# Kernel tuning notes

Measured on AMD Instinct MI355X. Metric: run time of the kernel, lower is better.

Reference implementation:

```python
import jax, jax.numpy as jnp
import numpy as np

B, S, D = 2, 2048, 1024   # batch, seq, token_dim
H, E = 16, 64             # heads, embedding_size per head


def setup_inputs() -> dict:
    key = jax.random.key(0)
    ks = jax.random.split(key, 5)
    x = jax.random.normal(ks[0], (B, S, D), dtype=jnp.float32)
    attention_mask = jnp.ones((B, S), dtype=jnp.int32)  # accepted but unused, as in source
    # torch.rand -> uniform [0,1)
    w_queries = jax.random.uniform(ks[1], (H, D, E), dtype=jnp.float32)
    w_keys = jax.random.uniform(ks[2], (H, D, E), dtype=jnp.float32)
    w_values = jax.random.uniform(ks[3], (H, D, E), dtype=jnp.float32)
    w_agg = jax.random.uniform(ks[4], (H * E, D), dtype=jnp.float32)
    return {"x": x, "attention_mask": attention_mask, "w_queries": w_queries,
            "w_keys": w_keys, "w_values": w_values, "w_agg": w_agg}


def reference(x, attention_mask, w_queries, w_keys, w_values, w_agg):
    # Batched over all heads at once (original loops in Python per head).
    q = jnp.einsum('bsd,hde->bhse', x, w_queries)  # [B,H,S,E]
    k = jnp.einsum('bsd,hde->bhse', x, w_keys)
    v = jnp.einsum('bsd,hde->bhse', x, w_values)
    scores = jnp.einsum('bhse,bhte->bhst', q, k) / jnp.sqrt(jnp.float32(E))  # [B,H,S,S]
    # NOTE: source applies softmax over dim=1 of the per-head [B,S,S] scores,
    # i.e. over the QUERY axis (axis=2 here), not the usual key axis.
    attn = jax.nn.softmax(scores, axis=2)
    heads = jnp.einsum('bhst,bhte->bhse', attn, v)  # [B,H,S,E]
    # concat along last dim in head order -> [B,S,H*E]
    multi = jnp.transpose(heads, (0, 2, 1, 3)).reshape(B, S, H * E)
    return multi @ w_agg  # [B,S,D]
```

## Files before the change

kernel.cpp:

```cpp
#include <hip/hip_runtime.h>
#include <hip/hip_bf16.h>


typedef __attribute__((ext_vector_type(8))) short bf16x8;
typedef __attribute__((ext_vector_type(4))) float f32x4;

#define C1 0.18033688011112042f

__device__ __forceinline__ unsigned short f2bf(float f){
  union { __hip_bfloat16 h; unsigned short u; } cv;
  cv.h = __float2bfloat16(f);
  return cv.u;
}
__device__ __forceinline__ unsigned int pk2(float a, float b){
  union { __hip_bfloat162 h; unsigned int u; } cv;
  cv.h = __float22bfloat162_rn(make_float2(a, b));
  return cv.u;
}
__device__ __forceinline__ unsigned long long pack4(float a, float b, float c, float d){
  return (unsigned long long)pk2(a, b) | ((unsigned long long)pk2(c, d) << 32);
}
__device__ __forceinline__ float bf2f(unsigned short u){
  unsigned int x = ((unsigned int)u) << 16;
  return __builtin_bit_cast(float, x);
}

__device__ __forceinline__ void swap32(unsigned a, unsigned b, unsigned &x, unsigned &y){
#if __has_builtin(__builtin_amdgcn_permlane32_swap)
  auto r = __builtin_amdgcn_permlane32_swap(a, b, false, false);
  x = r[0]; y = r[1];
#else
  int lane = threadIdx.x & 63;
  unsigned as = __shfl_xor((int)a, 32), bs = __shfl_xor((int)b, 32);
  x = (lane & 32) ? bs : a;
  y = (lane & 32) ? b : as;
#endif
}
__device__ __forceinline__ void swap16(unsigned a, unsigned b, unsigned &x, unsigned &y){
#if __has_builtin(__builtin_amdgcn_permlane16_swap)
  auto r = __builtin_amdgcn_permlane16_swap(a, b, false, false);
  x = r[0]; y = r[1];
#else
  int lane = threadIdx.x & 63;
  unsigned as = __shfl_xor((int)a, 16), bs = __shfl_xor((int)b, 16);
  x = (lane & 16) ? bs : a;
  y = (lane & 16) ? b : as;
#endif
}

#define GLOAD16(SRC, DST)                                                        \
  __builtin_amdgcn_global_load_lds(                                              \
      (const __attribute__((address_space(1))) void*)(SRC),                      \
      (__attribute__((address_space(3))) void*)(DST), 16, 0, 0)

__global__ void k_cvt_x(const float* __restrict__ in, unsigned short* __restrict__ out){
  int i = (blockIdx.x * 256 + threadIdx.x) * 4;
  float4 v = *reinterpret_cast<const float4*>(in + i);
  *reinterpret_cast<unsigned long long*>(out + i) = pack4(v.x, v.y, v.z, v.w);
}

__global__ __launch_bounds__(256) void k_cvt_w3t(const float* __restrict__ wq,
                                                 const float* __restrict__ wk,
                                                 const float* __restrict__ wv,
                                                 unsigned short* __restrict__ out){
  __shared__ unsigned short T[64][72];
  const int z = blockIdx.z;
  const float* w = ((z == 0) ? wq : ((z == 1) ? wk : wv)) + ((size_t)blockIdx.y << 16);
  const int d0 = blockIdx.x * 64;
  const int r = threadIdx.x >> 2, c0 = (threadIdx.x & 3) << 4;
  const float* src = w + ((size_t)(d0 + r) << 6) + c0;
#pragma unroll
  for (int i = 0; i < 4; ++i){
    float4 v = *(const float4*)(src + 4 * i);
    T[r][c0 + 4 * i + 0] = f2bf(v.x);
    T[r][c0 + 4 * i + 1] = f2bf(v.y);
    T[r][c0 + 4 * i + 2] = f2bf(v.z);
    T[r][c0 + 4 * i + 3] = f2bf(v.w);
  }
  __syncthreads();
  const int e = threadIdx.x >> 2, k0 = (threadIdx.x & 3) << 4;
  union { unsigned short s[8]; bf16x8 v; } u0, u1;
#pragma unroll
  for (int k = 0; k < 8; ++k){ u0.s[k] = T[k0 + k][e]; u1.s[k] = T[k0 + 8 + k][e]; }
  unsigned short* dst = out + ((size_t)z << 20) + (((size_t)blockIdx.y * 64 + e) << 10) + d0 + k0;
  *(bf16x8*)dst = u0.v;
  *(bf16x8*)(dst + 8) = u1.v;
}

__global__ __launch_bounds__(256) void k_cvt_waggt(const float* __restrict__ w,
                                                   unsigned short* __restrict__ out){
  __shared__ unsigned short T[64][72];
  const int d0 = blockIdx.x * 64, he0 = blockIdx.y * 64;
  const int r = threadIdx.x >> 2, c0 = (threadIdx.x & 3) << 4;
  const float* src = w + ((size_t)(he0 + r) << 10) + d0 + c0;
#pragma unroll
  for (int i = 0; i < 4; ++i){
    float4 v = *(const float4*)(src + 4 * i);
    T[r][c0 + 4 * i + 0] = f2bf(v.x);
    T[r][c0 + 4 * i + 1] = f2bf(v.y);
    T[r][c0 + 4 * i + 2] = f2bf(v.z);
    T[r][c0 + 4 * i + 3] = f2bf(v.w);
  }
  __syncthreads();
  const int d = threadIdx.x >> 2, k0 = (threadIdx.x & 3) << 4;
  union { unsigned short s[8]; bf16x8 v; } u0, u1;
#pragma unroll
  for (int k = 0; k < 8; ++k){ u0.s[k] = T[k0 + k][d]; u1.s[k] = T[k0 + 8 + k][d]; }
  unsigned short* dst = out + ((size_t)(d0 + d) << 11) + he0 + k0;
  *(bf16x8*)dst = u0.v;
  *(bf16x8*)(dst + 8) = u1.v;
  *(bf16x8*)(dst + 1024) = u0.v;
  *(bf16x8*)(dst + 1032) = u1.v;
}

__global__ __launch_bounds__(256) void k_proj(const unsigned short* __restrict__ Wall,
                                              const unsigned short* __restrict__ Xb,
                                              unsigned short* __restrict__ Qb,
                                              unsigned short* __restrict__ Kb,
                                              unsigned short* __restrict__ Vt){
  __shared__ __align__(16) unsigned short lds[2][2][4096];
  const int z = blockIdx.z;
  const unsigned short* Wt = Wall + ((size_t)z << 20);
  const int t = threadIdx.x;
  const int w = t >> 6, lane = t & 63, g = lane >> 4, cl = lane & 15;
  const int wn = w >> 1, wm = w & 1;
  const int n0 = blockIdx.x * 128, m0 = blockIdx.y * 128;

  const int rowS = t & 127;
  const unsigned short* sA = Wt + (size_t)(n0 + rowS) * 1024 + (t >> 7) * 8;
  const unsigned short* sB = Xb + (size_t)(m0 + rowS) * 1024 + (t >> 7) * 8;

  f32x4 acc[4][4];
#pragma unroll
  for (int i = 0; i < 4; ++i)
#pragma unroll
    for (int j = 0; j < 4; ++j) acc[i][j] = f32x4{0.f, 0.f, 0.f, 0.f};

  GLOAD16(sA,      &lds[0][0][t * 8]);
  GLOAD16(sA + 16, &lds[0][0][t * 8 + 2048]);
  GLOAD16(sB,      &lds[0][1][t * 8]);
  GLOAD16(sB + 16, &lds[0][1][t * 8 + 2048]);
  __syncthreads();

#pragma unroll 2
  for (int kt = 0; kt < 32; ++kt){
    const int cur = kt & 1;
    if (kt < 31){
      const unsigned short* nA = sA + (kt + 1) * 32;
      const unsigned short* nB = sB + (kt + 1) * 32;
      GLOAD16(nA,      &lds[cur ^ 1][0][t * 8]);
      GLOAD16(nA + 16, &lds[cur ^ 1][0][t * 8 + 2048]);
      GLOAD16(nB,      &lds[cur ^ 1][1][t * 8]);
      GLOAD16(nB + 16, &lds[cur ^ 1][1][t * 8 + 2048]);
    }
    const unsigned short* la = &lds[cur][0][g * 1024];
    const unsigned short* lb = &lds[cur][1][g * 1024];
    bf16x8 af[4], bq[4];
#pragma unroll
    for (int i = 0; i < 4; ++i) af[i] = *(const bf16x8*)(la + (wn * 64 + i * 16 + cl) * 8);
#pragma unroll
    for (int j = 0; j < 4; ++j) bq[j] = *(const bf16x8*)(lb + (wm * 64 + j * 16 + cl) * 8);
#pragma unroll
    for (int i = 0; i < 4; ++i)
#pragma unroll
      for (int j = 0; j < 4; ++j)
        acc[i][j] = __builtin_amdgcn_mfma_f32_16x16x32_bf16(af[i], bq[j], acc[i][j], 0, 0, 0);
    __syncthreads();
  }

  const float scale = (z == 0) ? C1 : 1.f;
#pragma unroll
  for (int i = 0; i < 4; ++i)
#pragma unroll
    for (int j = 0; j < 4; ++j)
#pragma unroll
      for (int jj = 0; jj < 4; ++jj) acc[i][j][jj] *= scale;

  if (z < 2){
    unsigned short* outp = (z == 0) ? Qb : Kb;
#pragma unroll
    for (int i = 0; i < 4; ++i)
#pragma unroll
      for (int j = 0; j < 4; ++j){
        int m = m0 + wm * 64 + 16 * j + cl;
        int n = n0 + wn * 64 + 16 * i + 4 * g;
        *reinterpret_cast<unsigned long long*>(outp + (size_t)m * 1024 + n) =
            pack4(acc[i][j][0], acc[i][j][1], acc[i][j][2], acc[i][j][3]);
      }
  } else {
    int b = m0 >> 11;
#pragma unroll
    for (int i = 0; i < 4; ++i)
#pragma unroll
      for (int j = 0; j < 4; ++j){
        int c2 = (m0 & 2047) + wm * 64 + 16 * j + cl;
        int nb = b * 1024 + n0 + wn * 64 + 16 * i + 4 * g;
#pragma unroll
        for (int jj = 0; jj < 4; ++jj)
          Vt[(size_t)(nb + jj) * 2048 + c2] = f2bf(acc[i][j][jj]);
      }
  }
}

__global__ __launch_bounds__(256) void k_agg(const unsigned short* __restrict__ Wa,
                                             const unsigned short* __restrict__ Hd,
                                             float* __restrict__ outp){
  __shared__ __align__(16) unsigned short lds[2][6144];
  const int t = threadIdx.x;
  const int w = t >> 6, lane = t & 63, g = lane >> 4, cl = lane & 15;
  const int wn = w >> 1, wm = w & 1;
  const int n0 = blockIdx.x * 64, m0 = blockIdx.y * 128;

  const unsigned short* sA  = Wa + (size_t)(n0 + (t & 63)) * 2048 + (t >> 6) * 8;
  const unsigned short* sB1 = Hd + (size_t)(m0 + (t & 127)) * 2048 + (t >> 7) * 8;
  unsigned short* dA0  = &lds[0][0]    + t * 8;
  unsigned short* dB10 = &lds[0][2048] + t * 8;

  f32x4 acc[2][4];
#pragma unroll
  for (int j = 0; j < 2; ++j)
#pragma unroll
    for (int i = 0; i < 4; ++i) acc[j][i] = f32x4{0.f, 0.f, 0.f, 0.f};

  GLOAD16(sA,       dA0);
  GLOAD16(sB1,      dB10);
  GLOAD16(sB1 + 16, dB10 + 2048);
  __syncthreads();

#pragma unroll 2
  for (int kt = 0; kt < 64; ++kt){
    const int cur = kt & 1;
    if (kt < 63){
      const unsigned short* nA = sA  + (kt + 1) * 32;
      const unsigned short* nB = sB1 + (kt + 1) * 32;
      GLOAD16(nA,      dA0  + (cur ^ 1) * 6144);
      GLOAD16(nB,      dB10 + (cur ^ 1) * 6144);
      GLOAD16(nB + 16, dB10 + (cur ^ 1) * 6144 + 2048);
    }
    const unsigned short* la = &lds[cur][0];
    const unsigned short* lb = &lds[cur][2048];
    bf16x8 af[2], bq[4];
#pragma unroll
    for (int j = 0; j < 2; ++j) af[j] = *(const bf16x8*)(la + g * 512 + (wn * 32 + j * 16 + cl) * 8);
#pragma unroll
    for (int i = 0; i < 4; ++i) bq[i] = *(const bf16x8*)(lb + g * 1024 + (wm * 64 + i * 16 + cl) * 8);
#pragma unroll
    for (int j = 0; j < 2; ++j)
#pragma unroll
      for (int i = 0; i < 4; ++i)
        acc[j][i] = __builtin_amdgcn_mfma_f32_16x16x32_bf16(af[j], bq[i], acc[j][i], 0, 0, 0);
    __syncthreads();
  }
#pragma unroll
  for (int j = 0; j < 2; ++j)
#pragma unroll
    for (int i = 0; i < 4; ++i){
      int m = m0 + wm * 64 + 16 * i + cl;
      int n = n0 + wn * 32 + 16 * j + 4 * g;
      *reinterpret_cast<f32x4*>(outp + (size_t)m * 1024 + n) = acc[j][i];
    }
}

__global__ __launch_bounds__(256, 4) void k_stats(const unsigned short* __restrict__ Qb,
                                                  const unsigned short* __restrict__ Kb,
                                                  float* __restrict__ mp,
                                                  float* __restrict__ lp){
  __shared__ __align__(16) unsigned short Qs[2][64][64];
  const int B = blockIdx.x;
  const int xcd = B & 7, rest = B >> 3;
  const int tx = rest & 7, gi = rest >> 3;
  const int grp = xcd + 8 * gi;
  const int bh = grp & 31, z = grp >> 5;
  const int b = bh >> 4, h = bh & 15;
  const int w = threadIdx.x >> 6, lane = threadIdx.x & 63;
  const int g = lane >> 4, cl = lane & 15;
  const int t0 = tx * 256 + w * 64;

  const unsigned short* kp = Kb + (size_t)(b * 2048 + t0 + cl) * 1024 + h * 64 + g * 8;
  bf16x8 a[4][2];
#pragma unroll
  for (int ti = 0; ti < 4; ++ti){
    a[ti][0] = *(const bf16x8*)(kp + (size_t)ti * 16 * 1024);
    a[ti][1] = *(const bf16x8*)(kp + (size_t)ti * 16 * 1024 + 32);
  }

  const int r0 = threadIdx.x >> 3, sl = threadIdx.x & 7;
  const unsigned short* qsrc = Qb + (size_t)(b * 2048 + z * 512 + r0) * 1024 + h * 64
                               + ((sl ^ (r0 & 7)) * 8);
  unsigned short* qdst0 = &Qs[0][0][0] + threadIdx.x * 8;

  const int e0 = (g ^ (cl & 7)) * 8;
  const int e1 = ((g + 4) ^ (cl & 7)) * 8;

  float m[16], l[16];
#pragma unroll
  for (int i = 0; i < 16; ++i){ m[i] = -3.0e38f; l[i] = 0.f; }

  GLOAD16(qsrc,             qdst0);
  GLOAD16(qsrc + 32 * 1024, qdst0 + 2048);
  __syncthreads();
  for (int c = 0; c < 8; ++c){
    const int buf = c & 1;
    if (c < 7){
      const unsigned short* s2 = qsrc + (size_t)(c + 1) * 64 * 1024;
      unsigned short* d2 = qdst0 + (buf ^ 1) * 4096;
      GLOAD16(s2,             d2);
      GLOAD16(s2 + 32 * 1024, d2 + 2048);
    }
#pragma unroll
    for (int st = 0; st < 4; ++st){
      const unsigned short* qrow = &Qs[buf][st * 16 + cl][0];
      bf16x8 b0 = *(const bf16x8*)(qrow + e0);
      bf16x8 b1 = *(const bf16x8*)(qrow + e1);
#pragma unroll
      for (int ti = 0; ti < 4; ++ti){
        f32x4 zz = {0.f, 0.f, 0.f, 0.f};
        f32x4 d = __builtin_amdgcn_mfma_f32_16x16x32_bf16(a[ti][0], b0, zz, 0, 0, 0);
        d = __builtin_amdgcn_mfma_f32_16x16x32_bf16(a[ti][1], b1, d, 0, 0, 0);
#pragma unroll
        for (int j = 0; j < 4; ++j) m[ti * 4 + j] = fmaxf(m[ti * 4 + j], d[j]);
      }
    }
    __syncthreads();
  }
#pragma unroll
  for (int off = 1; off < 16; off <<= 1)
#pragma unroll
    for (int i = 0; i < 16; ++i) m[i] = fmaxf(m[i], __shfl_xor(m[i], off));

  GLOAD16(qsrc,             qdst0);
  GLOAD16(qsrc + 32 * 1024, qdst0 + 2048);
  __syncthreads();
  for (int c = 0; c < 8; ++c){
    const int buf = c & 1;
    if (c < 7){
      const unsigned short* s2 = qsrc + (size_t)(c + 1) * 64 * 1024;
      unsigned short* d2 = qdst0 + (buf ^ 1) * 4096;
      GLOAD16(s2,             d2);
      GLOAD16(s2 + 32 * 1024, d2 + 2048);
    }
#pragma unroll
    for (int st = 0; st < 4; ++st){
      const unsigned short* qrow = &Qs[buf][st * 16 + cl][0];
      bf16x8 b0 = *(const bf16x8*)(qrow + e0);
      bf16x8 b1 = *(const bf16x8*)(qrow + e1);
#pragma unroll
      for (int ti = 0; ti < 4; ++ti){
        f32x4 zz = {0.f, 0.f, 0.f, 0.f};
        f32x4 d = __builtin_amdgcn_mfma_f32_16x16x32_bf16(a[ti][0], b0, zz, 0, 0, 0);
        d = __builtin_amdgcn_mfma_f32_16x16x32_bf16(a[ti][1], b1, d, 0, 0, 0);
#pragma unroll
        for (int j = 0; j < 4; ++j) l[ti * 4 + j] += exp2f(d[j] - m[ti * 4 + j]);
      }
    }
    __syncthreads();
  }
#pragma unroll
  for (int off = 1; off < 16; off <<= 1)
#pragma unroll
    for (int i = 0; i < 16; ++i) l[i] += __shfl_xor(l[i], off);

  if (cl == 0){
    size_t base = ((size_t)z * 32 + bh) * 2048 + t0;
#pragma unroll
    for (int ti = 0; ti < 4; ++ti){
      f32x4 mv = {m[ti * 4 + 0], m[ti * 4 + 1], m[ti * 4 + 2], m[ti * 4 + 3]};
      f32x4 lv = {l[ti * 4 + 0], l[ti * 4 + 1], l[ti * 4 + 2], l[ti * 4 + 3]};
      *(f32x4*)(mp + base + ti * 16 + 4 * g) = mv;
      *(f32x4*)(lp + base + ti * 16 + 4 * g) = lv;
    }
  }
}

__global__ void k_mcomb(const float* __restrict__ mp, const float* __restrict__ lp,
                        float* __restrict__ m2, float* __restrict__ rl){
  int i = blockIdx.x * 256 + threadIdx.x;
  float m0 = mp[i], m1 = mp[65536 + i], m2v = mp[131072 + i], m3 = mp[196608 + i];
  float l0 = lp[i], l1 = lp[65536 + i], l2 = lp[131072 + i], l3 = lp[196608 + i];
  float m = fmaxf(fmaxf(m0, m1), fmaxf(m2v, m3));
  float l = l0 * exp2f(m0 - m) + l1 * exp2f(m1 - m)
          + l2 * exp2f(m2v - m) + l3 * exp2f(m3 - m);
  m2[i] = m;
  rl[i] = 1.f / l;
}

__global__ void k_scale_v(unsigned short* __restrict__ Vt, const float* __restrict__ rl){
  int row = blockIdx.x;
  int b = row >> 10, h = (row >> 6) & 15;
  int t = threadIdx.x * 8;
  const float* r = rl + (size_t)(b * 16 + h) * 2048 + t;
  unsigned short* p = Vt + (size_t)row * 2048 + t;
  bf16x8 v = *(const bf16x8*)p;
  f32x4 r0 = *(const f32x4*)r;
  f32x4 r1 = *(const f32x4*)(r + 4);
  float f[8];
#pragma unroll
  for (int j = 0; j < 8; ++j) f[j] = bf2f((unsigned short)v[j]);
#pragma unroll
  for (int j = 0; j < 4; ++j){ f[j] *= r0[j]; f[4 + j] *= r1[j]; }
  unsigned long long* q = (unsigned long long*)p;
  q[0] = pack4(f[0], f[1], f[2], f[3]);
  q[1] = pack4(f[4], f[5], f[6], f[7]);
}

__global__ __launch_bounds__(256, 4) void k_attn(const unsigned short* __restrict__ Qb,
                                                 const unsigned short* __restrict__ Kb,
                                                 const unsigned short* __restrict__ Vt,
                                                 const float* __restrict__ m2,
                                                 unsigned short* __restrict__ Hd){
  __shared__ __align__(16) unsigned short KsL[2 * 64 * 64];
  __shared__ __align__(16) unsigned short VsL[2 * 64 * 64];
  __shared__ __align__(16) float Ms[1024];
  const int B = blockIdx.x;
  const int xcd = B & 7, rest = B >> 3;
  const int sx = rest & 15, gi = rest >> 4;
  const int grp = xcd + 8 * gi;
  const int bh = grp & 31, z = grp >> 5;
  const int b = bh >> 4, h = bh & 15;
  const int lane = threadIdx.x & 63;
  const int g = lane >> 4, cl = lane & 15;
  const int s0w = sx * 128 + (threadIdx.x >> 6) * 32;
  const int tbase = z * 1024;

  {
    int i = threadIdx.x * 4;
    *(f32x4*)&Ms[i] = *(const f32x4*)(m2 + (size_t)bh * 2048 + tbase + i);
  }

  bf16x8 q[2][2];
#pragma unroll
  for (int ss = 0; ss < 2; ++ss){
    const unsigned short* qp = Qb + (size_t)(b * 2048 + s0w + ss * 16 + cl) * 1024 + h * 64 + g * 8;
    q[ss][0] = *(const bf16x8*)(qp);
    q[ss][1] = *(const bf16x8*)(qp + 32);
  }
  f32x4 acc[4][2];
#pragma unroll
  for (int i = 0; i < 4; ++i)
#pragma unroll
    for (int ss = 0; ss < 2; ++ss) acc[i][ss] = f32x4{0.f, 0.f, 0.f, 0.f};

  const int srow = threadIdx.x >> 3;
  const int sseg = ((threadIdx.x & 7) ^ (srow & 7)) * 8;
  const unsigned short* kStage = Kb + (size_t)(b * 2048 + tbase + srow) * 1024 + h * 64 + sseg;
  const unsigned short* vStage = Vt + (size_t)(b * 1024 + h * 64 + srow) * 2048 + tbase + sseg;
  unsigned short* kDst = &KsL[0] + threadIdx.x * 8;
  unsigned short* vDst = &VsL[0] + threadIdx.x * 8;

  const int eK = (g ^ (cl & 7)) * 8;
  const int eK2 = ((g + 4) ^ (cl & 7)) * 8;

#define ASTAGE(c, buf) {                                                          \
    const unsigned short* ks_ = kStage + (size_t)(c) * 64 * 1024;                 \
    const unsigned short* vs_ = vStage + (c) * 64;                                \
    unsigned short* kd_ = kDst + (buf) * 4096;                                    \
    unsigned short* vd_ = vDst + (buf) * 4096;                                    \
    GLOAD16(ks_,             kd_);                                                \
    GLOAD16(ks_ + 32 * 1024, kd_ + 2048);                                         \
    GLOAD16(vs_,             vd_);                                                \
    GLOAD16(vs_ + (size_t)32 * 2048, vd_ + 2048); }

  ASTAGE(0, 0);
  __syncthreads();

  for (int c = 0; c < 16; ++c){
    const int buf = c & 1;
    if (c < 15) ASTAGE(c + 1, buf ^ 1);
    const unsigned short* Kbuf = &KsL[0] + buf * 4096;
    const unsigned short* Vbuf = &VsL[0] + buf * 4096;
#pragma unroll
    for (int sc = 0; sc < 2; ++sc){
      const unsigned short* kr0 = Kbuf + (sc * 32 + cl) * 64;
      const unsigned short* kr1 = Kbuf + (sc * 32 + 16 + cl) * 64;
      bf16x8 a00 = *(const bf16x8*)(kr0 + eK);
      bf16x8 a01 = *(const bf16x8*)(kr0 + eK2);
      bf16x8 a10 = *(const bf16x8*)(kr1 + eK);
      bf16x8 a11 = *(const bf16x8*)(kr1 + eK2);
      f32x4 mv0 = *(const f32x4*)&Ms[c * 64 + sc * 32 + 4 * g];
      f32x4 mv1 = *(const f32x4*)&Ms[c * 64 + sc * 32 + 16 + 4 * g];

      bf16x8 pb[2];
#pragma unroll
      for (int ss = 0; ss < 2; ++ss){
        f32x4 zz = {0.f, 0.f, 0.f, 0.f};
        __builtin_amdgcn_s_setprio(1);
        f32x4 d0 = __builtin_amdgcn_mfma_f32_16x16x32_bf16(a00, q[ss][0], zz, 0, 0, 0);
        d0 = __builtin_amdgcn_mfma_f32_16x16x32_bf16(a01, q[ss][1], d0, 0, 0, 0);
        f32x4 d1 = __builtin_amdgcn_mfma_f32_16x16x32_bf16(a10, q[ss][0], zz, 0, 0, 0);
        d1 = __builtin_amdgcn_mfma_f32_16x16x32_bf16(a11, q[ss][1], d1, 0, 0, 0);
        __builtin_amdgcn_s_setprio(0);
        unsigned w00 = pk2(exp2f(d0[0] - mv0[0]), exp2f(d0[1] - mv0[1]));
        unsigned w01 = pk2(exp2f(d0[2] - mv0[2]), exp2f(d0[3] - mv0[3]));
        unsigned w10 = pk2(exp2f(d1[0] - mv1[0]), exp2f(d1[1] - mv1[1]));
        unsigned w11 = pk2(exp2f(d1[2] - mv1[2]), exp2f(d1[3] - mv1[3]));
        unsigned sa0, sb0, sa1, sb1, W0, W1, W2, W3;
        swap32(w00, w10, sa0, sb0);
        swap32(w01, w11, sa1, sb1);
        swap16(sa0, sb0, W0, W2);
        swap16(sa1, sb1, W1, W3);
        union { unsigned u[4]; bf16x8 v; } fr;
        fr.u[0] = W0; fr.u[1] = W1; fr.u[2] = W2; fr.u[3] = W3;
        pb[ss] = fr.v;
      }
      __builtin_amdgcn_s_setprio(1);
#pragma unroll
      for (int i = 0; i < 4; ++i){
        bf16x8 av = *(const bf16x8*)(Vbuf + (16 * i + cl) * 64 + ((sc * 4 + g) ^ (cl & 7)) * 8);
        acc[i][0] = __builtin_amdgcn_mfma_f32_16x16x32_bf16(av, pb[0], acc[i][0], 0, 0, 0);
        acc[i][1] = __builtin_amdgcn_mfma_f32_16x16x32_bf16(av, pb[1], acc[i][1], 0, 0, 0);
      }
      __builtin_amdgcn_s_setprio(0);
    }
    __syncthreads();
  }
#undef ASTAGE
#pragma unroll
  for (int i = 0; i < 4; ++i)
#pragma unroll
    for (int ss = 0; ss < 2; ++ss){
      *reinterpret_cast<unsigned long long*>(
          Hd + (size_t)(b * 2048 + s0w + ss * 16 + cl) * 2048 + z * 1024 + h * 64 + 16 * i + 4 * g) =
          pack4(acc[i][ss][0], acc[i][ss][1], acc[i][ss][2], acc[i][ss][3]);
    }
}

extern "C" void kernel_launch(void* const* d_in, const int* in_sizes, int n_in,
                              void* d_out, int out_size, void* d_ws, size_t ws_size,
                              hipStream_t stream) {
  const float* x    = (const float*)d_in[0];
  const float* wq   = (const float*)d_in[2];
  const float* wk   = (const float*)d_in[3];
  const float* wv   = (const float*)d_in[4];
  const float* wagg = (const float*)d_in[5];
  float* outp = (float*)d_out;

  char* ws = (char*)d_ws;
  unsigned short* Xb  = (unsigned short*)(ws);
  unsigned short* Hd  = (unsigned short*)(ws);
  unsigned short* Wall= (unsigned short*)(ws + 16777216);
  float* mp = (float*)(ws + 16777216);
  float* lp = (float*)(ws + 17825792);
  float* m2 = (float*)(ws + 18874368);
  float* rl = (float*)(ws + 19136512);
  unsigned short* Wat = (unsigned short*)(ws + 23068672);
  unsigned short* Qb  = (unsigned short*)(ws + 27262976);
  unsigned short* Kb  = (unsigned short*)(ws + 35651584);
  unsigned short* Vt  = (unsigned short*)(ws + 44040192);

  k_cvt_x    <<<dim3(4096),       dim3(256), 0, stream>>>(x, Xb);
  k_cvt_w3t  <<<dim3(16, 16, 3),  dim3(256), 0, stream>>>(wq, wk, wv, Wall);
  k_cvt_waggt<<<dim3(16, 16),     dim3(256), 0, stream>>>(wagg, Wat);

  k_proj<<<dim3(8, 32, 3), dim3(256), 0, stream>>>(Wall, Xb, Qb, Kb, Vt);

  k_stats  <<<dim3(1024), dim3(256), 0, stream>>>(Qb, Kb, mp, lp);
  k_mcomb  <<<dim3(256),  dim3(256), 0, stream>>>(mp, lp, m2, rl);
  k_scale_v<<<dim3(2048), dim3(256), 0, stream>>>(Vt, rl);

  k_attn<<<dim3(1024), dim3(256), 0, stream>>>(Qb, Kb, Vt, m2, Hd);
  k_agg <<<dim3(16, 32), dim3(256), 0, stream>>>(Wat, Hd, outp);
}
```

Measured before the change: 245.4 us.

## Merge conversion kernels into one launch and fold max subtraction into MFMA accumulator

Combines the three fp32-to-bf16 conversion and transpose kernels into a single k_prep launch dispatched by block index, saving two kernel launches and the gaps between them. In the attention kernel, the softmax max is negated when loaded into shared memory and passed as the initial MFMA accumulator, so the subtraction happens inside the matrix op and is no longer a separate per-element subtract before exp2. The added branching in the merged prep kernel is small, but mixing block types in one grid may slightly change how work spreads across compute units.

```diff
diff --git a/kernel.cpp b/kernel.cpp
--- a/kernel.cpp
+++ b/kernel.cpp
@@ -53,64 +53,71 @@
       (const __attribute__((address_space(1))) void*)(SRC),                      \
       (__attribute__((address_space(3))) void*)(DST), 16, 0, 0)
 
-__global__ void k_cvt_x(const float* __restrict__ in, unsigned short* __restrict__ out){
-  int i = (blockIdx.x * 256 + threadIdx.x) * 4;
-  float4 v = *reinterpret_cast<const float4*>(in + i);
-  *reinterpret_cast<unsigned long long*>(out + i) = pack4(v.x, v.y, v.z, v.w);
-}
-
-__global__ __launch_bounds__(256) void k_cvt_w3t(const float* __restrict__ wq,
-                                                 const float* __restrict__ wk,
-                                                 const float* __restrict__ wv,
-                                                 unsigned short* __restrict__ out){
+__global__ __launch_bounds__(256) void k_prep(const float* __restrict__ x,
+                                              const float* __restrict__ wq,
+                                              const float* __restrict__ wk,
+                                              const float* __restrict__ wv,
+                                              const float* __restrict__ wagg,
+                                              unsigned short* __restrict__ Xb,
+                                              unsigned short* __restrict__ Wall,
+                                              unsigned short* __restrict__ Wat){
   __shared__ unsigned short T[64][72];
-  const int z = blockIdx.z;
-  const float* w = ((z == 0) ? wq : ((z == 1) ? wk : wv)) + ((size_t)blockIdx.y << 16);
-  const int d0 = blockIdx.x * 64;
+  int bid = blockIdx.x;
+  if (bid < 4096){
+    int i = (bid * 256 + threadIdx.x) * 4;
+    float4 v = *reinterpret_cast<const float4*>(x + i);
+    *reinterpret_cast<unsigned long long*>(Xb + i) = pack4(v.x, v.y, v.z, v.w);
+    return;
+  }
+  bid -= 4096;
   const int r = threadIdx.x >> 2, c0 = (threadIdx.x & 3) << 4;
-  const float* src = w + ((size_t)(d0 + r) << 6) + c0;
-#pragma unroll
-  for (int i = 0; i < 4; ++i){
-    float4 v = *(const float4*)(src + 4 * i);
-    T[r][c0 + 4 * i + 0] = f2bf(v.x);
-    T[r][c0 + 4 * i + 1] = f2bf(v.y);
-    T[r][c0 + 4 * i + 2] = f2bf(v.z);
-    T[r][c0 + 4 * i + 3] = f2bf(v.w);
-  }
-  __syncthreads();
-  const int e = threadIdx.x >> 2, k0 = (threadIdx.x & 3) << 4;
-  union { unsigned short s[8]; bf16x8 v; } u0, u1;
-#pragma unroll
-  for (int k = 0; k < 8; ++k){ u0.s[k] = T[k0 + k][e]; u1.s[k] = T[k0 + 8 + k][e]; }
-  unsigned short* dst = out + ((size_t)z << 20) + (((size_t)blockIdx.y * 64 + e) << 10) + d0 + k0;
-  *(bf16x8*)dst = u0.v;
-  *(bf16x8*)(dst + 8) = u1.v;
-}
-
-__global__ __launch_bounds__(256) void k_cvt_waggt(const float* __restrict__ w,
-                                                   unsigned short* __restrict__ out){
-  __shared__ unsigned short T[64][72];
-  const int d0 = blockIdx.x * 64, he0 = blockIdx.y * 64;
-  const int r = threadIdx.x >> 2, c0 = (threadIdx.x & 3) << 4;
-  const float* src = w + ((size_t)(he0 + r) << 10) + d0 + c0;
-#pragma unroll
-  for (int i = 0; i < 4; ++i){
-    float4 v = *(const float4*)(src + 4 * i);
-    T[r][c0 + 4 * i + 0] = f2bf(v.x);
-    T[r][c0 + 4 * i + 1] = f2bf(v.y);
-    T[r][c0 + 4 * i + 2] = f2bf(v.z);
-    T[r][c0 + 4 * i + 3] = f2bf(v.w);
-  }
-  __syncthreads();
-  const int d = threadIdx.x >> 2, k0 = (threadIdx.x & 3) << 4;
-  union { unsigned short s[8]; bf16x8 v; } u0, u1;
-#pragma unroll
-  for (int k = 0; k < 8; ++k){ u0.s[k] = T[k0 + k][d]; u1.s[k] = T[k0 + 8 + k][d]; }
-  unsigned short* dst = out + ((size_t)(d0 + d) << 11) + he0 + k0;
-  *(bf16x8*)dst = u0.v;
-  *(bf16x8*)(dst + 8) = u1.v;
-  *(bf16x8*)(dst + 1024) = u0.v;
-  *(bf16x8*)(dst + 1032) = u1.v;
+  if (bid < 768){
+    const int z = bid >> 8, rem = bid & 255, hy = rem >> 4, dt = rem & 15;
+    const float* w = ((z == 0) ? wq : ((z == 1) ? wk : wv)) + ((size_t)hy << 16);
+    const int d0 = dt * 64;
+    const float* src = w + ((size_t)(d0 + r) << 6) + c0;
+#pragma unroll
+    for (int i = 0; i < 4; ++i){
+      float4 v = *(const float4*)(src + 4 * i);
+      T[r][c0 + 4 * i + 0] = f2bf(v.x);
+      T[r][c0 + 4 * i + 1] = f2bf(v.y);
+      T[r][c0 + 4 * i + 2] = f2bf(v.z);
+      T[r][c0 + 4 * i + 3] = f2bf(v.w);
+    }
+    __syncthreads();
+    const int e = threadIdx.x >> 2, k0 = (threadIdx.x & 3) << 4;
+    union { unsigned short s[8]; bf16x8 v; } u0, u1;
+#pragma unroll
+    for (int k = 0; k < 8; ++k){ u0.s[k] = T[k0 + k][e]; u1.s[k] = T[k0 + 8 + k][e]; }
+    unsigned short* dst = Wall + ((size_t)z << 20) + (((size_t)hy * 64 + e) << 10) + d0 + k0;
+    *(bf16x8*)dst = u0.v;
+    *(bf16x8*)(dst + 8) = u1.v;
+    return;
+  }
+  bid -= 768;
+  {
+    const int het = bid >> 4, dt = bid & 15;
+    const int d0 = dt * 64, he0 = het * 64;
+    const float* src = wagg + ((size_t)(he0 + r) << 10) + d0 + c0;
+#pragma unroll
+    for (int i = 0; i < 4; ++i){
+      float4 v = *(const float4*)(src + 4 * i);
+      T[r][c0 + 4 * i + 0] = f2bf(v.x);
+      T[r][c0 + 4 * i + 1] = f2bf(v.y);
+      T[r][c0 + 4 * i + 2] = f2bf(v.z);
+      T[r][c0 + 4 * i + 3] = f2bf(v.w);
+    }
+    __syncthreads();
+    const int d = threadIdx.x >> 2, k0 = (threadIdx.x & 3) << 4;
+    union { unsigned short s[8]; bf16x8 v; } u0, u1;
+#pragma unroll
+    for (int k = 0; k < 8; ++k){ u0.s[k] = T[k0 + k][d]; u1.s[k] = T[k0 + 8 + k][d]; }
+    unsigned short* dst = Wat + ((size_t)(d0 + d) << 11) + he0 + k0;
+    *(bf16x8*)dst = u0.v;
+    *(bf16x8*)(dst + 8) = u1.v;
+    *(bf16x8*)(dst + 1024) = u0.v;
+    *(bf16x8*)(dst + 1032) = u1.v;
+  }
 }
 
 __global__ __launch_bounds__(256) void k_proj(const unsigned short* __restrict__ Wall,
@@ -424,7 +431,8 @@
 
   {
     int i = threadIdx.x * 4;
-    *(f32x4*)&Ms[i] = *(const f32x4*)(m2 + (size_t)bh * 2048 + tbase + i);
+    f32x4 mv = *(const f32x4*)(m2 + (size_t)bh * 2048 + tbase + i);
+    *(f32x4*)&Ms[i] = f32x4{-mv[0], -mv[1], -mv[2], -mv[3]};
   }
 
   bf16x8 q[2][2];
@@ -476,23 +484,22 @@
       bf16x8 a01 = *(const bf16x8*)(kr0 + eK2);
       bf16x8 a10 = *(const bf16x8*)(kr1 + eK);
       bf16x8 a11 = *(const bf16x8*)(kr1 + eK2);
-      f32x4 mv0 = *(const f32x4*)&Ms[c * 64 + sc * 32 + 4 * g];
-      f32x4 mv1 = *(const f32x4*)&Ms[c * 64 + sc * 32 + 16 + 4 * g];
+      f32x4 ci0 = *(const f32x4*)&Ms[c * 64 + sc * 32 + 4 * g];
+      f32x4 ci1 = *(const f32x4*)&Ms[c * 64 + sc * 32 + 16 + 4 * g];
 
       bf16x8 pb[2];
 #pragma unroll
       for (int ss = 0; ss < 2; ++ss){
-        f32x4 zz = {0.f, 0.f, 0.f, 0.f};
         __builtin_amdgcn_s_setprio(1);
-        f32x4 d0 = __builtin_amdgcn_mfma_f32_16x16x32_bf16(a00, q[ss][0], zz, 0, 0, 0);
+        f32x4 d0 = __builtin_amdgcn_mfma_f32_16x16x32_bf16(a00, q[ss][0], ci0, 0, 0, 0);
         d0 = __builtin_amdgcn_mfma_f32_16x16x32_bf16(a01, q[ss][1], d0, 0, 0, 0);
-        f32x4 d1 = __builtin_amdgcn_mfma_f32_16x16x32_bf16(a10, q[ss][0], zz, 0, 0, 0);
+        f32x4 d1 = __builtin_amdgcn_mfma_f32_16x16x32_bf16(a10, q[ss][0], ci1, 0, 0, 0);
         d1 = __builtin_amdgcn_mfma_f32_16x16x32_bf16(a11, q[ss][1], d1, 0, 0, 0);
         __builtin_amdgcn_s_setprio(0);
-        unsigned w00 = pk2(exp2f(d0[0] - mv0[0]), exp2f(d0[1] - mv0[1]));
-        unsigned w01 = pk2(exp2f(d0[2] - mv0[2]), exp2f(d0[3] - mv0[3]));
-        unsigned w10 = pk2(exp2f(d1[0] - mv1[0]), exp2f(d1[1] - mv1[1]));
-        unsigned w11 = pk2(exp2f(d1[2] - mv1[2]), exp2f(d1[3] - mv1[3]));
+        unsigned w00 = pk2(exp2f(d0[0]), exp2f(d0[1]));
+        unsigned w01 = pk2(exp2f(d0[2]), exp2f(d0[3]));
+        unsigned w10 = pk2(exp2f(d1[0]), exp2f(d1[1]));
+        unsigned w11 = pk2(exp2f(d1[2]), exp2f(d1[3]));
         unsigned sa0, sb0, sa1, sb1, W0, W1, W2, W3;
         swap32(w00, w10, sa0, sb0);
         swap32(w01, w11, sa1, sb1);
@@ -547,9 +554,7 @@
   unsigned short* Kb  = (unsigned short*)(ws + 35651584);
   unsigned short* Vt  = (unsigned short*)(ws + 44040192);
 
-  k_cvt_x    <<<dim3(4096),       dim3(256), 0, stream>>>(x, Xb);
-  k_cvt_w3t  <<<dim3(16, 16, 3),  dim3(256), 0, stream>>>(wq, wk, wv, Wall);
-  k_cvt_waggt<<<dim3(16, 16),     dim3(256), 0, stream>>>(wagg, Wat);
+  k_prep<<<dim3(5120), dim3(256), 0, stream>>>(x, wq, wk, wv, wagg, Xb, Wall, Wat);
 
   k_proj<<<dim3(8, 32, 3), dim3(256), 0, stream>>>(Wall, Xb, Qb, Kb, Vt);
 
```

Measured after the change: 239.1 us, median of 2. 2.6% less time.
